# Kernel optimization log

Hardware: AMD Instinct MI355X
Metric: run time of the kernel (lower is better)

## Reference

```python
import jax, jax.numpy as jnp
import numpy as np

THRESHOLD = 0.15


def _level(Tf, Sf, g, threshold):
    # Tf, g: [B, C_t, H, W]  (detached in original); Sf: [B, C_s, H, W]
    B = Tf.shape[0]
    Tf = jax.lax.stop_gradient(Tf)
    g = jax.lax.stop_gradient(g)
    # GradCAM channel weights: mean of gradient over spatial dims -> [B, C]
    w = jnp.mean(g, axis=(2, 3))
    # weighted sum over channels -> cam [B, H, W]
    cam = jnp.einsum('bc,bchw->bhw', w, Tf)
    # threshold from pre-clamp max (as in original code order)
    thresh = jnp.max(cam.reshape(B, -1), axis=1) * threshold  # [B]
    cam = jnp.clip(cam, 0.0)
    score = jnp.mean(cam, axis=(1, 2))  # [B]
    mask = cam > jnp.abs(thresh)[:, None, None]  # [B, H, W]
    # per-sample channel-mean at masked spatial points; zeros elsewhere
    embT = jnp.where(mask, jnp.mean(Tf, axis=1), 0.0).reshape(B, -1)
    embS = jnp.where(mask, jnp.mean(Sf, axis=1), 0.0).reshape(B, -1)
    return score, embT, embS


def setup_inputs() -> dict:
    key = jax.random.key(0)
    k = jax.random.split(key, 6)
    B = 32
    return {
        'Tf0': jax.random.normal(k[0], (B, 512, 38, 38), jnp.float32),
        'Tf1': jax.random.normal(k[1], (B, 1024, 19, 19), jnp.float32),
        'Sf0': jax.random.normal(k[2], (B, 512, 38, 38), jnp.float32),
        'Sf1': jax.random.normal(k[3], (B, 1024, 19, 19), jnp.float32),
        'g0': jax.random.normal(k[4], (B, 512, 38, 38), jnp.float32),
        'g1': jax.random.normal(k[5], (B, 1024, 19, 19), jnp.float32),
    }


def reference(Tf0, Tf1, Sf0, Sf1, g0, g1):
    s0, embT0, embS0 = _level(Tf0, Sf0, g0, THRESHOLD)
    s1, embT1, embS1 = _level(Tf1, Sf1, g1, THRESHOLD)
    # feature_weight: [B, n_levels] -> sum over batch, normalize over levels
    fw = jnp.stack([s0, s1], axis=1).sum(axis=0)
    fw = fw / jnp.sum(fw)
    return fw, embT0, embT1, embS0, embS1
```

## Files before the change

### kernel.cpp

```cpp
#include <hip/hip_runtime.h>
#include <math.h>

#define BB   32
#define C0   512
#define HW0  1444
#define C1   1024
#define HW1  361
#define THRS 0.15f

#define CHUNKS0 12
#define CHUNKS1 12

__global__ void k_weights(const float* __restrict__ g0,
                          const float* __restrict__ g1,
                          float* __restrict__ w0,
                          float* __restrict__ w1) {
    int bid  = blockIdx.x;
    int tid  = threadIdx.x;
    int wv   = tid >> 6;
    int lane = tid & 63;
    float sum = 0.f;
    int level0 = (bid < 4096);
    int row;
    if (level0) {
        row = bid * 4 + wv;
        const float4* p4 = (const float4*)(g0 + (size_t)row * HW0);
        for (int i = lane; i < HW0 / 4; i += 64) {
            float4 v = p4[i];
            sum += (v.x + v.y) + (v.z + v.w);
        }
    } else {
        row = (bid - 4096) * 4 + wv;
        const float* p = g1 + (size_t)row * HW1;
        for (int i = lane; i < HW1; i += 64) sum += p[i];
    }
    #pragma unroll
    for (int off = 32; off > 0; off >>= 1) sum += __shfl_down(sum, off, 64);
    if (lane == 0) {
        if (level0) w0[row] = sum * (1.0f / HW0);
        else        w1[row] = sum * (1.0f / HW1);
    }
}

__global__ void k_cam(const float* __restrict__ Tf0, const float* __restrict__ Sf0,
                      const float* __restrict__ Tf1, const float* __restrict__ Sf1,
                      const float* __restrict__ w0,  const float* __restrict__ w1,
                      float* __restrict__ cam0, float* __restrict__ cam1,
                      float* __restrict__ outT0, float* __restrict__ outS0,
                      float* __restrict__ outT1, float* __restrict__ outS1) {
    __shared__ float  wsh[C1];
    __shared__ float4 red[3][256];

    int bid = blockIdx.x;
    int tid = threadIdx.x;
    int cg = tid >> 5, lane = tid & 31;

    if (bid < BB * CHUNKS0) {
        int b = bid / CHUNKS0, chunk = bid % CHUNKS0;
        for (int i = tid; i < C0; i += 256) wsh[i] = w0[b * C0 + i];
        __syncthreads();

        int hw = chunk * 128 + lane * 4;
        float4 camA = {0,0,0,0}, tA = {0,0,0,0}, sA = {0,0,0,0};
        if (hw < HW0) {
            size_t base = ((size_t)b * C0 + (size_t)cg * 64) * HW0 + hw;
            const float* pT = Tf0 + base;
            const float* pS = Sf0 + base;
            const float* pw = wsh + cg * 64;
            #pragma unroll 4
            for (int i = 0; i < 64; ++i) {
                float4 tv = *(const float4*)(pT + (size_t)i * HW0);
                float4 sv = *(const float4*)(pS + (size_t)i * HW0);
                float wc = pw[i];
                camA.x += wc * tv.x; camA.y += wc * tv.y;
                camA.z += wc * tv.z; camA.w += wc * tv.w;
                tA.x += tv.x; tA.y += tv.y; tA.z += tv.z; tA.w += tv.w;
                sA.x += sv.x; sA.y += sv.y; sA.z += sv.z; sA.w += sv.w;
            }
        }
        red[0][tid] = camA; red[1][tid] = tA; red[2][tid] = sA;
        __syncthreads();
        for (int s = 128; s >= 32; s >>= 1) {
            if (tid < s) {
                #pragma unroll
                for (int a = 0; a < 3; ++a) {
                    float4 x = red[a][tid], y = red[a][tid + s];
                    x.x += y.x; x.y += y.y; x.z += y.z; x.w += y.w;
                    red[a][tid] = x;
                }
            }
            __syncthreads();
        }
        if (tid < 32 && (chunk * 128 + tid * 4) < HW0) {
            size_t o = (size_t)b * HW0 + chunk * 128 + tid * 4;
            float4 c4 = red[0][tid], t4 = red[1][tid], s4 = red[2][tid];
            *(float4*)(cam0 + o) = c4;
            const float invC = 1.0f / C0;
            float2 tlo = {t4.x * invC, t4.y * invC}, thi = {t4.z * invC, t4.w * invC};
            float2 slo = {s4.x * invC, s4.y * invC}, shi = {s4.z * invC, s4.w * invC};
            *(float2*)(outT0 + o)     = tlo;
            *(float2*)(outT0 + o + 2) = thi;
            *(float2*)(outS0 + o)     = slo;
            *(float2*)(outS0 + o + 2) = shi;
        }
    } else {
        int id = bid - BB * CHUNKS0;
        int b = id / CHUNKS1, chunk = id % CHUNKS1;
        for (int i = tid; i < C1; i += 256) wsh[i] = w1[b * C1 + i];
        __syncthreads();

        int hw = chunk * 32 + lane;
        float camAcc = 0.f, tAcc = 0.f, sAcc = 0.f;
        if (hw < HW1) {
            size_t base = ((size_t)b * C1 + (size_t)cg * 128) * HW1 + hw;
            const float* pT = Tf1 + base;
            const float* pS = Sf1 + base;
            const float* pw = wsh + cg * 128;
            #pragma unroll 4
            for (int i = 0; i < 128; ++i) {
                float tv = pT[(size_t)i * HW1];
                float sv = pS[(size_t)i * HW1];
                camAcc += pw[i] * tv;
                tAcc   += tv;
                sAcc   += sv;
            }
        }
        red[0][tid].x = camAcc; red[1][tid].x = tAcc; red[2][tid].x = sAcc;
        __syncthreads();
        for (int s = 128; s >= 32; s >>= 1) {
            if (tid < s) {
                red[0][tid].x += red[0][tid + s].x;
                red[1][tid].x += red[1][tid + s].x;
                red[2][tid].x += red[2][tid + s].x;
            }
            __syncthreads();
        }
        if (tid < 32 && (chunk * 32 + tid) < HW1) {
            const float invC = 1.0f / C1;
            size_t o = (size_t)b * HW1 + chunk * 32 + tid;
            cam1[o]  = red[0][tid].x;
            outT1[o] = red[1][tid].x * invC;
            outS1[o] = red[2][tid].x * invC;
        }
    }
}

__global__ void k_mask(const float* __restrict__ cam0, const float* __restrict__ cam1,
                       float* __restrict__ outT0, float* __restrict__ outS0,
                       float* __restrict__ outT1, float* __restrict__ outS1,
                       float* __restrict__ score) {
    int bid = blockIdx.x;
    const float* cam; float *outT, *outS, *sc; int HW, b;
    if (bid < BB) { cam = cam0; outT = outT0; outS = outS0; HW = HW0; b = bid;      sc = score; }
    else          { cam = cam1; outT = outT1; outS = outS1; HW = HW1; b = bid - BB; sc = score + BB; }
    int tid = threadIdx.x;
    const float* camb = cam + (size_t)b * HW;

    float m = -INFINITY, s = 0.f;
    for (int i = tid; i < HW; i += 256) {
        float c = camb[i];
        m = fmaxf(m, c);
        s += fmaxf(c, 0.f);
    }
    #pragma unroll
    for (int off = 32; off > 0; off >>= 1) {
        m = fmaxf(m, __shfl_down(m, off, 64));
        s += __shfl_down(s, off, 64);
    }
    __shared__ float rm[4], rs[4];
    __shared__ float bm;
    if ((tid & 63) == 0) { rm[tid >> 6] = m; rs[tid >> 6] = s; }
    __syncthreads();
    if (tid == 0) {
        float mm = fmaxf(fmaxf(rm[0], rm[1]), fmaxf(rm[2], rm[3]));
        float ss = (rs[0] + rs[1]) + (rs[2] + rs[3]);
        bm = mm;
        sc[b] = ss / (float)HW;
    }
    __syncthreads();
    float athr = fabsf(bm * THRS);
    float* oT = outT + (size_t)b * HW;
    float* oS = outS + (size_t)b * HW;
    for (int i = tid; i < HW; i += 256) {
        float c = fmaxf(camb[i], 0.f);
        if (!(c > athr)) { oT[i] = 0.f; oS[i] = 0.f; }
    }
}

__global__ void k_fw(const float* __restrict__ score, float* __restrict__ out) {
    int tid = threadIdx.x;
    float v = score[tid];
    #pragma unroll
    for (int off = 16; off > 0; off >>= 1) v += __shfl_down(v, off, 32);
    __shared__ float sh[2];
    if ((tid & 31) == 0) sh[tid >> 5] = v;
    __syncthreads();
    if (tid == 0) {
        float t = sh[0] + sh[1];
        out[0] = sh[0] / t;
        out[1] = sh[1] / t;
    }
}

extern "C" void kernel_launch(void* const* d_in, const int* in_sizes, int n_in,
                              void* d_out, int out_size, void* d_ws, size_t ws_size,
                              hipStream_t stream) {
    const float* Tf0 = (const float*)d_in[0];
    const float* Tf1 = (const float*)d_in[1];
    const float* Sf0 = (const float*)d_in[2];
    const float* Sf1 = (const float*)d_in[3];
    const float* g0  = (const float*)d_in[4];
    const float* g1  = (const float*)d_in[5];

    float* out   = (float*)d_out;
    float* fw    = out;
    float* outT0 = out + 2;
    float* outT1 = outT0 + BB * HW0;
    float* outS0 = outT1 + BB * HW1;
    float* outS1 = outS0 + BB * HW0;

    float* ws    = (float*)d_ws;
    float* w0    = ws;
    float* w1    = w0 + BB * C0;
    float* cam0  = w1 + BB * C1;
    float* cam1  = cam0 + BB * HW0;
    float* score = cam1 + BB * HW1;

    k_weights<<<4096 + 8192, 256, 0, stream>>>(g0, g1, w0, w1);
    k_cam<<<BB * CHUNKS0 + BB * CHUNKS1, 256, 0, stream>>>(
        Tf0, Sf0, Tf1, Sf1, w0, w1, cam0, cam1, outT0, outS0, outT1, outS1);
    k_mask<<<2 * BB, 256, 0, stream>>>(cam0, cam1, outT0, outS0, outT1, outS1, score);
    k_fw<<<1, 64, 0, stream>>>(score, fw);
}
```

Baseline: 380.9 us.

## Split channel reduction in cam kernel across blocks, finish in mask kernel

The cam kernel now splits each channel range into four parts, so it launches four times as many blocks and each thread runs a shorter loop. Each block writes partial cam, T-sum and S-sum values to workspace. The mask kernel sums the four partials in shared memory, then applies scaling and masking and writes the outputs directly. This aims to raise occupancy and memory parallelism on the bandwidth-bound channel reduction, at the cost of extra partial-buffer traffic and more shared memory in the mask kernel.

```diff
diff --git a/kernel.cpp b/kernel.cpp
--- a/kernel.cpp
+++ b/kernel.cpp
@@ -10,6 +10,7 @@
 
 #define CHUNKS0 12
 #define CHUNKS1 12
+#define SPLIT   4
 
 __global__ void k_weights(const float* __restrict__ g0,
                           const float* __restrict__ g1,
@@ -45,30 +46,31 @@
 __global__ void k_cam(const float* __restrict__ Tf0, const float* __restrict__ Sf0,
                       const float* __restrict__ Tf1, const float* __restrict__ Sf1,
                       const float* __restrict__ w0,  const float* __restrict__ w1,
-                      float* __restrict__ cam0, float* __restrict__ cam1,
-                      float* __restrict__ outT0, float* __restrict__ outS0,
-                      float* __restrict__ outT1, float* __restrict__ outS1) {
-    __shared__ float  wsh[C1];
+                      float* __restrict__ camP0, float* __restrict__ tP0, float* __restrict__ sP0,
+                      float* __restrict__ camP1, float* __restrict__ tP1, float* __restrict__ sP1) {
+    __shared__ float  wsh[256];
     __shared__ float4 red[3][256];
 
     int bid = blockIdx.x;
     int tid = threadIdx.x;
     int cg = tid >> 5, lane = tid & 31;
 
-    if (bid < BB * CHUNKS0) {
-        int b = bid / CHUNKS0, chunk = bid % CHUNKS0;
-        for (int i = tid; i < C0; i += 256) wsh[i] = w0[b * C0 + i];
+    if (bid < BB * CHUNKS0 * SPLIT) {
+        int b = bid / (CHUNKS0 * SPLIT);
+        int rem = bid % (CHUNKS0 * SPLIT);
+        int chunk = rem >> 2, part = rem & 3;
+        if (tid < 128) wsh[tid] = w0[b * C0 + part * 128 + tid];
         __syncthreads();
 
         int hw = chunk * 128 + lane * 4;
         float4 camA = {0,0,0,0}, tA = {0,0,0,0}, sA = {0,0,0,0};
         if (hw < HW0) {
-            size_t base = ((size_t)b * C0 + (size_t)cg * 64) * HW0 + hw;
+            size_t base = ((size_t)b * C0 + (size_t)part * 128 + (size_t)cg * 16) * HW0 + hw;
             const float* pT = Tf0 + base;
             const float* pS = Sf0 + base;
-            const float* pw = wsh + cg * 64;
-            #pragma unroll 4
-            for (int i = 0; i < 64; ++i) {
+            const float* pw = wsh + cg * 16;
+            #pragma unroll
+            for (int i = 0; i < 16; ++i) {
                 float4 tv = *(const float4*)(pT + (size_t)i * HW0);
                 float4 sv = *(const float4*)(pS + (size_t)i * HW0);
                 float wc = pw[i];
@@ -92,32 +94,28 @@
             __syncthreads();
         }
         if (tid < 32 && (chunk * 128 + tid * 4) < HW0) {
-            size_t o = (size_t)b * HW0 + chunk * 128 + tid * 4;
-            float4 c4 = red[0][tid], t4 = red[1][tid], s4 = red[2][tid];
-            *(float4*)(cam0 + o) = c4;
-            const float invC = 1.0f / C0;
-            float2 tlo = {t4.x * invC, t4.y * invC}, thi = {t4.z * invC, t4.w * invC};
-            float2 slo = {s4.x * invC, s4.y * invC}, shi = {s4.z * invC, s4.w * invC};
-            *(float2*)(outT0 + o)     = tlo;
-            *(float2*)(outT0 + o + 2) = thi;
-            *(float2*)(outS0 + o)     = slo;
-            *(float2*)(outS0 + o + 2) = shi;
+            size_t o = ((size_t)part * BB + b) * HW0 + chunk * 128 + tid * 4;
+            *(float4*)(camP0 + o) = red[0][tid];
+            *(float4*)(tP0   + o) = red[1][tid];
+            *(float4*)(sP0   + o) = red[2][tid];
         }
     } else {
-        int id = bid - BB * CHUNKS0;
-        int b = id / CHUNKS1, chunk = id % CHUNKS1;
-        for (int i = tid; i < C1; i += 256) wsh[i] = w1[b * C1 + i];
+        int id = bid - BB * CHUNKS0 * SPLIT;
+        int b = id / (CHUNKS1 * SPLIT);
+        int rem = id % (CHUNKS1 * SPLIT);
+        int chunk = rem >> 2, part = rem & 3;
+        wsh[tid] = w1[b * C1 + part * 256 + tid];
         __syncthreads();
 
         int hw = chunk * 32 + lane;
         float camAcc = 0.f, tAcc = 0.f, sAcc = 0.f;
         if (hw < HW1) {
-            size_t base = ((size_t)b * C1 + (size_t)cg * 128) * HW1 + hw;
+            size_t base = ((size_t)b * C1 + (size_t)part * 256 + (size_t)cg * 32) * HW1 + hw;
             const float* pT = Tf1 + base;
             const float* pS = Sf1 + base;
-            const float* pw = wsh + cg * 128;
-            #pragma unroll 4
-            for (int i = 0; i < 128; ++i) {
+            const float* pw = wsh + cg * 32;
+            #pragma unroll 8
+            for (int i = 0; i < 32; ++i) {
                 float tv = pT[(size_t)i * HW1];
                 float sv = pS[(size_t)i * HW1];
                 camAcc += pw[i] * tv;
@@ -136,29 +134,47 @@
             __syncthreads();
         }
         if (tid < 32 && (chunk * 32 + tid) < HW1) {
-            const float invC = 1.0f / C1;
-            size_t o = (size_t)b * HW1 + chunk * 32 + tid;
-            cam1[o]  = red[0][tid].x;
-            outT1[o] = red[1][tid].x * invC;
-            outS1[o] = red[2][tid].x * invC;
-        }
-    }
-}
-
-__global__ void k_mask(const float* __restrict__ cam0, const float* __restrict__ cam1,
+            size_t o = ((size_t)part * BB + b) * HW1 + chunk * 32 + tid;
+            camP1[o] = red[0][tid].x;
+            tP1[o]   = red[1][tid].x;
+            sP1[o]   = red[2][tid].x;
+        }
+    }
+}
+
+__global__ void k_mask(const float* __restrict__ camP0, const float* __restrict__ tP0,
+                       const float* __restrict__ sP0,
+                       const float* __restrict__ camP1, const float* __restrict__ tP1,
+                       const float* __restrict__ sP1,
                        float* __restrict__ outT0, float* __restrict__ outS0,
                        float* __restrict__ outT1, float* __restrict__ outS1,
                        float* __restrict__ score) {
+    __shared__ float camL[HW0], tL[HW0], sL[HW0];
+    __shared__ float rm[4], rs[4], bm;
+
     int bid = blockIdx.x;
-    const float* cam; float *outT, *outS, *sc; int HW, b;
-    if (bid < BB) { cam = cam0; outT = outT0; outS = outS0; HW = HW0; b = bid;      sc = score; }
-    else          { cam = cam1; outT = outT1; outS = outS1; HW = HW1; b = bid - BB; sc = score + BB; }
     int tid = threadIdx.x;
-    const float* camb = cam + (size_t)b * HW;
+    const float *camP, *tP, *sP; float *outT, *outS, *sc;
+    int HW, b; float invC;
+    if (bid < BB) {
+        camP = camP0; tP = tP0; sP = sP0; outT = outT0; outS = outS0;
+        HW = HW0; b = bid; sc = score; invC = 1.0f / C0;
+    } else {
+        camP = camP1; tP = tP1; sP = sP1; outT = outT1; outS = outS1;
+        HW = HW1; b = bid - BB; sc = score + BB; invC = 1.0f / C1;
+    }
+    size_t strideP = (size_t)BB * HW;
+    size_t base = (size_t)b * HW;
 
     float m = -INFINITY, s = 0.f;
     for (int i = tid; i < HW; i += 256) {
-        float c = camb[i];
+        float c = camP[base + i] + camP[strideP + base + i]
+                + camP[2 * strideP + base + i] + camP[3 * strideP + base + i];
+        float t = tP[base + i] + tP[strideP + base + i]
+                + tP[2 * strideP + base + i] + tP[3 * strideP + base + i];
+        float v = sP[base + i] + sP[strideP + base + i]
+                + sP[2 * strideP + base + i] + sP[3 * strideP + base + i];
+        camL[i] = c; tL[i] = t; sL[i] = v;
         m = fmaxf(m, c);
         s += fmaxf(c, 0.f);
     }
@@ -167,8 +183,6 @@
         m = fmaxf(m, __shfl_down(m, off, 64));
         s += __shfl_down(s, off, 64);
     }
-    __shared__ float rm[4], rs[4];
-    __shared__ float bm;
     if ((tid & 63) == 0) { rm[tid >> 6] = m; rs[tid >> 6] = s; }
     __syncthreads();
     if (tid == 0) {
@@ -179,11 +193,11 @@
     }
     __syncthreads();
     float athr = fabsf(bm * THRS);
-    float* oT = outT + (size_t)b * HW;
-    float* oS = outS + (size_t)b * HW;
     for (int i = tid; i < HW; i += 256) {
-        float c = fmaxf(camb[i], 0.f);
-        if (!(c > athr)) { oT[i] = 0.f; oS[i] = 0.f; }
+        float c = fmaxf(camL[i], 0.f);
+        bool keep = (c > athr);
+        outT[base + i] = keep ? tL[i] * invC : 0.f;
+        outS[base + i] = keep ? sL[i] * invC : 0.f;
     }
 }
 
@@ -222,13 +236,18 @@
     float* ws    = (float*)d_ws;
     float* w0    = ws;
     float* w1    = w0 + BB * C0;
-    float* cam0  = w1 + BB * C1;
-    float* cam1  = cam0 + BB * HW0;
-    float* score = cam1 + BB * HW1;
+    float* camP0 = w1 + BB * C1;
+    float* tP0   = camP0 + SPLIT * BB * HW0;
+    float* sP0   = tP0   + SPLIT * BB * HW0;
+    float* camP1 = sP0   + SPLIT * BB * HW0;
+    float* tP1   = camP1 + SPLIT * BB * HW1;
+    float* sP1   = tP1   + SPLIT * BB * HW1;
+    float* score = sP1   + SPLIT * BB * HW1;
 
     k_weights<<<4096 + 8192, 256, 0, stream>>>(g0, g1, w0, w1);
-    k_cam<<<BB * CHUNKS0 + BB * CHUNKS1, 256, 0, stream>>>(
-        Tf0, Sf0, Tf1, Sf1, w0, w1, cam0, cam1, outT0, outS0, outT1, outS1);
-    k_mask<<<2 * BB, 256, 0, stream>>>(cam0, cam1, outT0, outS0, outT1, outS1, score);
+    k_cam<<<BB * CHUNKS0 * SPLIT + BB * CHUNKS1 * SPLIT, 256, 0, stream>>>(
+        Tf0, Sf0, Tf1, Sf1, w0, w1, camP0, tP0, sP0, camP1, tP1, sP1);
+    k_mask<<<2 * BB, 256, 0, stream>>>(camP0, tP0, sP0, camP1, tP1, sP1,
+                                       outT0, outS0, outT1, outS1, score);
     k_fw<<<1, 64, 0, stream>>>(score, fw);
 }
```

Result: no change. 379.1 us (-0.5%).
